# Performance work log

Measured on AMD Instinct MI355X. Metric: run time of the kernel, lower is better.

## Reference

```python
import jax, jax.numpy as jnp
import numpy as np
import math

DIM = 1024
NUM_HEADS = 16
SHARED_HEADS = 1
ROUTED_HEADS = 3
HEAD_DIM = DIM // NUM_HEADS
B, N = 2, 2048


def setup_inputs() -> dict:
    key = jax.random.key(0)
    ks = jax.random.split(key, 16)
    s = 1.0 / math.sqrt(DIM)
    inp = {
        "x": jax.random.normal(ks[0], (B, N, DIM), dtype=jnp.float32),
        "Wq": jax.random.uniform(ks[1], (DIM, DIM), minval=-s, maxval=s),
        "bq": jax.random.uniform(ks[2], (DIM,), minval=-s, maxval=s),
        "Wk": jax.random.uniform(ks[3], (DIM, DIM), minval=-s, maxval=s),
        "bk": jax.random.uniform(ks[4], (DIM,), minval=-s, maxval=s),
        "Wv": jax.random.uniform(ks[5], (DIM, DIM), minval=-s, maxval=s),
        "bv": jax.random.uniform(ks[6], (DIM,), minval=-s, maxval=s),
        "Wp": jax.random.uniform(ks[7], (DIM, DIM), minval=-s, maxval=s),
        "bp": jax.random.uniform(ks[8], (DIM,), minval=-s, maxval=s),
        "Wr": jax.random.uniform(ks[9], (NUM_HEADS - SHARED_HEADS, DIM), minval=-s, maxval=s),
        "br": jax.random.uniform(ks[10], (NUM_HEADS - SHARED_HEADS,), minval=-s, maxval=s),
        "Ws": jax.random.uniform(ks[11], (2, DIM), minval=-s, maxval=s),
        "bs": jax.random.uniform(ks[12], (2,), minval=-s, maxval=s),
        # temperature init: log(exp(1/0.24)-1), shape (H,1,1)
        "temperature": jnp.full((NUM_HEADS, 1, 1), float(np.log(np.expm1(1.0 / 0.24))), dtype=jnp.float32),
        "query_embedding": 0.02 * jax.random.normal(ks[13], (NUM_HEADS, 1, HEAD_DIM), dtype=jnp.float32),
    }
    return inp


def reference(x, Wq, bq, Wk, bk, Wv, bv, Wp, bp, Wr, br, Ws, bs, temperature, query_embedding):
    Bsz, Nn, C = x.shape
    H, hd = NUM_HEADS, HEAD_DIM

    def heads(W, b):
        y = x @ W.T + b  # [B,N,C]
        return y.reshape(Bsz, Nn, H, hd).transpose(0, 2, 1, 3)  # [B,H,N,hd]

    q = heads(Wq, bq)
    k = heads(Wk, bk)
    v = heads(Wv, bv)

    q_norm = q / jnp.linalg.norm(q, axis=-1, keepdims=True)
    q_scaled = (q_norm + query_embedding[None]) * jax.nn.softplus(temperature)[None]
    attn = jnp.einsum("bhqd,bhkd->bhqk", q_scaled, k) / math.sqrt(hd)
    attn = jax.nn.softmax(attn, axis=-1)
    h = jnp.einsum("bhqk,bhkd->bhqd", attn, v)
    h = h.transpose(0, 2, 1, 3).reshape(Bsz, Nn, C)  # [B,N,C]

    # routed-head gating
    gates = jax.nn.softmax(h @ Wr.T + br, axis=-1)  # [B,N,H-shared]
    _, idx = jax.lax.top_k(gates, ROUTED_HEADS)
    # NOTE: original uses num_classes=num_heads-shared_heads for one_hot
    mask = jax.nn.one_hot(idx, H - SHARED_HEADS, dtype=gates.dtype).sum(axis=-2)
    routed_gates = gates * mask * ROUTED_HEADS

    sw = jax.nn.softmax(h @ Ws.T + bs, axis=-1)  # [B,N,2]
    shared_gates = sw * SHARED_HEADS
    weight_0 = sw * 2.0
    shared_gates = weight_0[..., 0:1] * shared_gates
    routed_gates = weight_0[..., 1:2] * routed_gates
    masked_gates = jnp.concatenate([shared_gates, routed_gates], axis=-1)

    # einsum('bnc,bnd->bnd') == per-token scalar sum over c times h
    out = h * masked_gates.sum(axis=-1, keepdims=True)
    return out @ Wp.T + bp
```

## Files before the change

kernel.cpp:

```cpp
#include <hip/hip_runtime.h>
#include <hip/hip_bf16.h>

typedef short s16x8 __attribute__((ext_vector_type(8)));
typedef float f32x4 __attribute__((ext_vector_type(4)));

__device__ __forceinline__ float b2f(unsigned short u) {
    union { unsigned int i; float f; } v;
    v.i = ((unsigned int)u) << 16;
    return v.f;
}
__device__ __forceinline__ unsigned short f2b(float f) {
    unsigned int x = __builtin_bit_cast(unsigned int, f);
    unsigned int r = (x + 0x7fffu + ((x >> 16) & 1u)) >> 16;
    return (unsigned short)r;
}
__device__ __forceinline__ unsigned int pkbf16(float a, float b) {
    union { __hip_bfloat162 h; unsigned int u; } v;
    v.h = __float22bfloat162_rn(make_float2(a, b));
    return v.u;
}
__device__ __forceinline__ float fast_exp2(float x) { return exp2f(x); }

__device__ __forceinline__ void gl_lds16(const unsigned short* g, unsigned short* l) {
    __builtin_amdgcn_global_load_lds(
        (const __attribute__((address_space(1))) void*)g,
        (__attribute__((address_space(3))) void*)l, 16, 0, 0);
}


__device__ __forceinline__ void cvt8(const float* __restrict__ s,
                                     unsigned short* __restrict__ d, int i) {
    const float* p = s + (size_t)i * 8;
    float4 a = *(const float4*)p;
    float4 b = *(const float4*)(p + 4);
    unsigned int u0 = pkbf16(a.x, a.y), u1 = pkbf16(a.z, a.w);
    unsigned int u2 = pkbf16(b.x, b.y), u3 = pkbf16(b.z, b.w);
    uint4 o = {u0, u1, u2, u3};
    *(uint4*)&d[(size_t)i * 8] = o;
}

__global__ __launch_bounds__(256) void cvt_main(
    const float* __restrict__ x,  const float* __restrict__ Wq,
    const float* __restrict__ Wk, const float* __restrict__ Wv,
    const float* __restrict__ Wr, const float* __restrict__ Ws,
    const float* __restrict__ bq, const float* __restrict__ bk,
    const float* __restrict__ bv,
    unsigned short* __restrict__ xb, unsigned short* __restrict__ wqkv,
    unsigned short* __restrict__ wg, float* __restrict__ bqkv)
{
    int blk = blockIdx.x, t = threadIdx.x;
    if (blk < 2048)      cvt8(x,  xb,             blk * 256 + t);
    else if (blk < 2560) cvt8(Wq, wqkv,           (blk - 2048) * 256 + t);
    else if (blk < 3072) cvt8(Wk, wqkv + 1048576, (blk - 2560) * 256 + t);
    else if (blk < 3584) cvt8(Wv, wqkv + 2097152, (blk - 3072) * 256 + t);
    else if (blk < 3592) { int i = (blk - 3584) * 256 + t; if (i < 1920) cvt8(Wr, wg, i); }
    else if (blk < 3593) { int i = t; cvt8(Ws, wg + 15360, i); }
    else {
        int i = (blk - 3593) * 256 + t;
        bqkv[i] = (i < 1024) ? bq[i] : (i < 2048) ? bk[i - 1024] : bv[i - 2048];
    }
}

__global__ __launch_bounds__(256) void cvt_kernel(
    const float* __restrict__ src, unsigned short* __restrict__ dst, int n8)
{
    int i = blockIdx.x * 256 + threadIdx.x;
    if (i < n8) cvt8(src, dst, i);
}

__global__ __launch_bounds__(256) void qkv_gemm(
    const unsigned short* __restrict__ A,
    const unsigned short* __restrict__ Bw,
    const float* __restrict__ bias,
    unsigned short* __restrict__ Q, unsigned short* __restrict__ K,
    unsigned short* __restrict__ Vt)
{
    __shared__ __attribute__((aligned(16))) unsigned short As[128 * 64];
    __shared__ __attribute__((aligned(16))) unsigned short Bs[128 * 64];
    const int t = threadIdx.x;
    const int wave = t >> 6, lane = t & 63;
    const int m0 = blockIdx.x * 128, n0 = blockIdx.y * 128;
    const int wm = (wave >> 1) * 64, wn = (wave & 1) * 64;
    const int lr = lane & 15, lq = lane >> 4;
    const int srow = lane >> 3;
    const int scol = (((lane & 7) ^ srow) << 3);

    f32x4 acc[4][4];
#pragma unroll
    for (int i = 0; i < 4; ++i)
#pragma unroll
        for (int j = 0; j < 4; ++j) acc[i][j] = (f32x4){0.f, 0.f, 0.f, 0.f};

    for (int k0 = 0; k0 < 1024; k0 += 64) {
        __syncthreads();
#pragma unroll
        for (int i = 0; i < 4; ++i) {
            int rb = wave * 32 + i * 8;
            gl_lds16(&A[(size_t)(m0 + rb + srow) * 1024 + k0 + scol], &As[rb * 64]);
            gl_lds16(&Bw[(size_t)(n0 + rb + srow) * 1024 + k0 + scol], &Bs[rb * 64]);
        }
        __syncthreads();
#pragma unroll
        for (int kk = 0; kk < 64; kk += 32) {
            const int po = ((((kk >> 3) + lq) ^ (lr & 7)) << 3);
            s16x8 af[4], bf[4];
#pragma unroll
            for (int i = 0; i < 4; ++i)
                af[i] = *(const s16x8*)&As[(wm + i * 16 + lr) * 64 + po];
#pragma unroll
            for (int j = 0; j < 4; ++j)
                bf[j] = *(const s16x8*)&Bs[(wn + j * 16 + lr) * 64 + po];
#pragma unroll
            for (int i = 0; i < 4; ++i)
#pragma unroll
                for (int j = 0; j < 4; ++j)
                    acc[i][j] = __builtin_amdgcn_mfma_f32_16x16x32_bf16(af[i], bf[j], acc[i][j], 0, 0, 0);
        }
    }
    const int kind = n0 >> 10;
    const int nc = n0 & 1023;
    if (kind < 2) {
        unsigned short* Cm = kind ? K : Q;
#pragma unroll
        for (int j = 0; j < 4; ++j) {
            int cl = wn + j * 16 + lr;
            float bv = bias[n0 + cl];
#pragma unroll
            for (int i = 0; i < 4; ++i) {
                int rowb = m0 + wm + i * 16 + lq * 4;
                unsigned int u0 = pkbf16(acc[i][j][0] + bv, acc[i][j][1] + bv);
                unsigned int u1 = pkbf16(acc[i][j][2] + bv, acc[i][j][3] + bv);
                Cm[(size_t)(rowb + 0) * 1024 + nc + cl] = (unsigned short)u0;
                Cm[(size_t)(rowb + 1) * 1024 + nc + cl] = (unsigned short)(u0 >> 16);
                Cm[(size_t)(rowb + 2) * 1024 + nc + cl] = (unsigned short)u1;
                Cm[(size_t)(rowb + 3) * 1024 + nc + cl] = (unsigned short)(u1 >> 16);
            }
        }
    } else {
        const int bb = m0 >> 11;
#pragma unroll
        for (int j = 0; j < 4; ++j) {
            int col = nc + wn + j * 16 + lr;
            int hh = col >> 6, dd = col & 63;
            float bv = bias[n0 + wn + j * 16 + lr];
#pragma unroll
            for (int i = 0; i < 4; ++i) {
                int tokb = m0 + wm + i * 16 + lq * 4;
                int tloc = tokb & 2047;
                uint2 u;
                u.x = pkbf16(acc[i][j][0] + bv, acc[i][j][1] + bv);
                u.y = pkbf16(acc[i][j][2] + bv, acc[i][j][3] + bv);
                *(uint2*)&Vt[((size_t)(bb * 16 + hh) * 64 + dd) * 2048 + tloc] = u;
            }
        }
    }
}

__global__ __launch_bounds__(256) void attn_kernel(
    const unsigned short* __restrict__ Q,
    const unsigned short* __restrict__ Kb,
    const unsigned short* __restrict__ Vt,
    const float* __restrict__ temp,
    const float* __restrict__ qe,
    unsigned short* __restrict__ Hout)
{
    __shared__ __attribute__((aligned(16))) unsigned short Qs[64 * 64];
    __shared__ __attribute__((aligned(16))) unsigned short Ks[64 * 64];
    __shared__ __attribute__((aligned(16))) unsigned short Vs[64 * 64];
    __shared__ __attribute__((aligned(16))) unsigned short Ps[64 * 72];
    const int t = threadIdx.x, wave = t >> 6, lane = t & 63;
    const int lr = lane & 15, lq = lane >> 4;
    const int bh = blockIdx.y, b = bh >> 4, h = bh & 15;
    const int q0 = blockIdx.x * 64;
    const int srow = lane >> 3;
    const int scol = (((lane & 7) ^ srow) << 3);

#pragma unroll
    for (int i = 0; i < 2; ++i) {
        int rb = wave * 16 + i * 8;
        gl_lds16(&Q[(size_t)(b * 2048 + q0 + rb + srow) * 1024 + h * 64 + scol], &Qs[rb * 64]);
    }
    __syncthreads();

    {
        const int qr = t >> 2, part = t & 3;
        const int pb0 = (((part * 2) ^ (qr & 7)) << 3);
        const int pb1 = (((part * 2 + 1) ^ (qr & 7)) << 3);
        s16x8 a = *(const s16x8*)&Qs[qr * 64 + pb0];
        s16x8 c = *(const s16x8*)&Qs[qr * 64 + pb1];
        float va[8], vc[8];
        float ss = 0.f;
#pragma unroll
        for (int e = 0; e < 8; ++e) {
            va[e] = b2f((unsigned short)a[e]); vc[e] = b2f((unsigned short)c[e]);
            ss += va[e] * va[e] + vc[e] * vc[e];
        }
        ss += __shfl_xor(ss, 1); ss += __shfl_xor(ss, 2);
        float rn = rsqrtf(ss);
        float tv = temp[h];
        float sp = ((tv > 20.f) ? tv : log1pf(__expf(tv))) * 0.18033688f;
        const float* qh = qe + h * 64 + part * 16;
        s16x8 oa, oc;
#pragma unroll
        for (int e = 0; e < 8; e += 2) {
            unsigned int u0 = pkbf16((va[e] * rn + qh[e]) * sp, (va[e + 1] * rn + qh[e + 1]) * sp);
            unsigned int u1 = pkbf16((vc[e] * rn + qh[8 + e]) * sp, (vc[e + 1] * rn + qh[8 + e + 1]) * sp);
            oa[e] = (short)u0; oa[e + 1] = (short)(u0 >> 16);
            oc[e] = (short)u1; oc[e + 1] = (short)(u1 >> 16);
        }
        *(s16x8*)&Qs[qr * 64 + pb0] = oa;
        *(s16x8*)&Qs[qr * 64 + pb1] = oc;
    }

    f32x4 accO[4];
#pragma unroll
    for (int j = 0; j < 4; ++j) accO[j] = (f32x4){0.f, 0.f, 0.f, 0.f};
    float lsum[4] = {0.f, 0.f, 0.f, 0.f};

    for (int kc = 0; kc < 2048; kc += 64) {
        __syncthreads();
#pragma unroll
        for (int i = 0; i < 2; ++i) {
            int rb = wave * 16 + i * 8;
            gl_lds16(&Kb[(size_t)(b * 2048 + kc + rb + srow) * 1024 + h * 64 + scol], &Ks[rb * 64]);
            gl_lds16(&Vt[((size_t)(b * 16 + h) * 64 + rb + srow) * 2048 + kc + scol], &Vs[rb * 64]);
        }
        __syncthreads();

        f32x4 s[4];
#pragma unroll
        for (int j = 0; j < 4; ++j) s[j] = (f32x4){0.f, 0.f, 0.f, 0.f};
#pragma unroll
        for (int kk = 0; kk < 64; kk += 32) {
            const int po = ((((kk >> 3) + lq) ^ (lr & 7)) << 3);
            s16x8 aq = *(const s16x8*)&Qs[(wave * 16 + lr) * 64 + po];
#pragma unroll
            for (int j = 0; j < 4; ++j) {
                s16x8 bk = *(const s16x8*)&Ks[(j * 16 + lr) * 64 + po];
                s[j] = __builtin_amdgcn_mfma_f32_16x16x32_bf16(aq, bk, s[j], 0, 0, 0);
            }
        }

#pragma unroll
        for (int r = 0; r < 4; ++r) {
            float p0 = fast_exp2(s[0][r]), p1 = fast_exp2(s[1][r]);
            float p2 = fast_exp2(s[2][r]), p3 = fast_exp2(s[3][r]);
            lsum[r] += (p0 + p1) + (p2 + p3);
            unsigned int ua = pkbf16(p0, p1), ub = pkbf16(p2, p3);
            int base = (wave * 16 + lq * 4 + r) * 72 + lr;
            Ps[base]      = (unsigned short)ua;
            Ps[base + 16] = (unsigned short)(ua >> 16);
            Ps[base + 32] = (unsigned short)ub;
            Ps[base + 48] = (unsigned short)(ub >> 16);
        }

#pragma unroll
        for (int kk = 0; kk < 64; kk += 32) {
            const int po = ((((kk >> 3) + lq) ^ (lr & 7)) << 3);
            s16x8 ap = *(const s16x8*)&Ps[(wave * 16 + lr) * 72 + kk + lq * 8];
#pragma unroll
            for (int j = 0; j < 4; ++j) {
                s16x8 bv = *(const s16x8*)&Vs[(j * 16 + lr) * 64 + po];
                accO[j] = __builtin_amdgcn_mfma_f32_16x16x32_bf16(ap, bv, accO[j], 0, 0, 0);
            }
        }
    }

#pragma unroll
    for (int r = 0; r < 4; ++r) {
        float l = lsum[r];
        l += __shfl_xor(l, 1); l += __shfl_xor(l, 2);
        l += __shfl_xor(l, 4); l += __shfl_xor(l, 8);
        float inv = 1.f / l;
        int row = q0 + wave * 16 + lq * 4 + r;
        size_t ob = (size_t)(b * 2048 + row) * 1024 + h * 64 + lr;
        unsigned int u0 = pkbf16(accO[0][r] * inv, accO[1][r] * inv);
        unsigned int u1 = pkbf16(accO[2][r] * inv, accO[3][r] * inv);
        Hout[ob]      = (unsigned short)u0;
        Hout[ob + 16] = (unsigned short)(u0 >> 16);
        Hout[ob + 32] = (unsigned short)u1;
        Hout[ob + 48] = (unsigned short)(u1 >> 16);
    }
}

__global__ __launch_bounds__(256) void gl_gemm(
    const unsigned short* __restrict__ Hb,
    const unsigned short* __restrict__ Wg,
    float* __restrict__ logits)
{
    __shared__ __attribute__((aligned(16))) unsigned short As[128 * 64];
    __shared__ __attribute__((aligned(16))) unsigned short Gs[32 * 64];
    const int t = threadIdx.x, wave = t >> 6, lane = t & 63;
    const int lr = lane & 15, lq = lane >> 4;
    const int m0 = blockIdx.x * 128;
    const int srow = lane >> 3;
    const int scol = (((lane & 7) ^ srow) << 3);

    f32x4 acc[2][2];
#pragma unroll
    for (int i = 0; i < 2; ++i)
#pragma unroll
        for (int j = 0; j < 2; ++j) acc[i][j] = (f32x4){0.f, 0.f, 0.f, 0.f};

    for (int k0 = 0; k0 < 1024; k0 += 64) {
        __syncthreads();
#pragma unroll
        for (int i = 0; i < 4; ++i) {
            int rb = wave * 32 + i * 8;
            gl_lds16(&Hb[(size_t)(m0 + rb + srow) * 1024 + k0 + scol], &As[rb * 64]);
        }
        {
            int row = wave * 8 + srow;
            int wr = (row > 16) ? 16 : row;
            gl_lds16(&Wg[(size_t)wr * 1024 + k0 + scol], &Gs[wave * 8 * 64]);
        }
        __syncthreads();
#pragma unroll
        for (int kk = 0; kk < 64; kk += 32) {
            const int po = ((((kk >> 3) + lq) ^ (lr & 7)) << 3);
            s16x8 af[2], gf[2];
#pragma unroll
            for (int i = 0; i < 2; ++i)
                af[i] = *(const s16x8*)&As[(wave * 32 + i * 16 + lr) * 64 + po];
#pragma unroll
            for (int j = 0; j < 2; ++j)
                gf[j] = *(const s16x8*)&Gs[(j * 16 + lr) * 64 + po];
#pragma unroll
            for (int i = 0; i < 2; ++i)
#pragma unroll
                for (int j = 0; j < 2; ++j)
                    acc[i][j] = __builtin_amdgcn_mfma_f32_16x16x32_bf16(af[i], gf[j], acc[i][j], 0, 0, 0);
        }
    }
#pragma unroll
    for (int i = 0; i < 2; ++i)
#pragma unroll
        for (int j = 0; j < 2; ++j) {
            int col = j * 16 + lr;
            int rowb = m0 + wave * 32 + i * 16 + lq * 4;
#pragma unroll
            for (int r = 0; r < 4; ++r)
                logits[(size_t)(rowb + r) * 32 + col] = acc[i][j][r];
        }
}

__global__ __launch_bounds__(256) void gate_apply(
    unsigned short* __restrict__ Hb,
    const float* __restrict__ logits,
    const float* __restrict__ br,
    const float* __restrict__ bs)
{
    const int tok = blockIdx.x, t = threadIdx.x;
    float lg[17];
#pragma unroll
    for (int j = 0; j < 17; ++j)
        lg[j] = logits[(size_t)tok * 32 + j] + ((j < 15) ? br[j] : bs[j - 15]);
    float mx = lg[0];
#pragma unroll
    for (int j = 1; j < 15; ++j) mx = fmaxf(mx, lg[j]);
    float sum = 0.f, v1 = -1.f, v2 = -1.f, v3 = -1.f;
#pragma unroll
    for (int j = 0; j < 15; ++j) {
        float e = __expf(lg[j] - mx);
        sum += e;
        if (e > v1)      { v3 = v2; v2 = v1; v1 = e; }
        else if (e > v2) { v3 = v2; v2 = e; }
        else if (e > v3) { v3 = e; }
    }
    float tops = (v1 + v2 + v3) / sum;
    float sm = fmaxf(lg[15], lg[16]);
    float e0 = __expf(lg[15] - sm), e1 = __expf(lg[16] - sm);
    float inv = 1.f / (e0 + e1);
    float g = 2.f * (e0 * inv) + 6.f * (e1 * inv) * tops;

    size_t base = (size_t)tok * 1024 + t * 4;
    ushort4 hr = *(const ushort4*)&Hb[base];
    unsigned int u0 = pkbf16(b2f(hr.x) * g, b2f(hr.y) * g);
    unsigned int u1 = pkbf16(b2f(hr.z) * g, b2f(hr.w) * g);
    uint2 o = {u0, u1};
    *(uint2*)&Hb[base] = o;
}

__global__ __launch_bounds__(256) void gemm64_out(
    const unsigned short* __restrict__ A,
    const unsigned short* __restrict__ Bw,
    const float* __restrict__ bias,
    float* __restrict__ C)
{
    __shared__ __attribute__((aligned(16))) unsigned short As[64 * 64];
    __shared__ __attribute__((aligned(16))) unsigned short Bs[128 * 64];
    const int t = threadIdx.x, wave = t >> 6, lane = t & 63;
    const int lr = lane & 15, lq = lane >> 4;
    const int m0 = blockIdx.x * 64, n0 = blockIdx.y * 128;
    const int wm = (wave >> 1) * 32, wn = (wave & 1) * 64;
    const int srow = lane >> 3;
    const int scol = (((lane & 7) ^ srow) << 3);

    f32x4 acc[2][4];
#pragma unroll
    for (int i = 0; i < 2; ++i)
#pragma unroll
        for (int j = 0; j < 4; ++j) acc[i][j] = (f32x4){0.f, 0.f, 0.f, 0.f};

    for (int k0 = 0; k0 < 1024; k0 += 64) {
        __syncthreads();
#pragma unroll
        for (int i = 0; i < 2; ++i) {
            int rb = wave * 16 + i * 8;
            gl_lds16(&A[(size_t)(m0 + rb + srow) * 1024 + k0 + scol], &As[rb * 64]);
        }
#pragma unroll
        for (int i = 0; i < 4; ++i) {
            int rb = wave * 32 + i * 8;
            gl_lds16(&Bw[(size_t)(n0 + rb + srow) * 1024 + k0 + scol], &Bs[rb * 64]);
        }
        __syncthreads();
#pragma unroll
        for (int kk = 0; kk < 64; kk += 32) {
            const int po = ((((kk >> 3) + lq) ^ (lr & 7)) << 3);
            s16x8 af[2], bf[4];
#pragma unroll
            for (int i = 0; i < 2; ++i)
                af[i] = *(const s16x8*)&As[(wm + i * 16 + lr) * 64 + po];
#pragma unroll
            for (int j = 0; j < 4; ++j)
                bf[j] = *(const s16x8*)&Bs[(wn + j * 16 + lr) * 64 + po];
#pragma unroll
            for (int i = 0; i < 2; ++i)
#pragma unroll
                for (int j = 0; j < 4; ++j)
                    acc[i][j] = __builtin_amdgcn_mfma_f32_16x16x32_bf16(af[i], bf[j], acc[i][j], 0, 0, 0);
        }
    }
#pragma unroll
    for (int j = 0; j < 4; ++j) {
        int col = n0 + wn + j * 16 + lr;
        float bv = bias[col];
#pragma unroll
        for (int i = 0; i < 2; ++i) {
            int rowb = m0 + wm + i * 16 + lq * 4;
#pragma unroll
            for (int r = 0; r < 4; ++r)
                C[(size_t)(rowb + r) * 1024 + col] = acc[i][j][r] + bv;
        }
    }
}

extern "C" void kernel_launch(void* const* d_in, const int* in_sizes, int n_in,
                              void* d_out, int out_size, void* d_ws, size_t ws_size,
                              hipStream_t stream)
{
    (void)in_sizes; (void)n_in; (void)out_size; (void)ws_size;
    const float* x   = (const float*)d_in[0];
    const float* Wq  = (const float*)d_in[1];
    const float* bq  = (const float*)d_in[2];
    const float* Wk  = (const float*)d_in[3];
    const float* bk  = (const float*)d_in[4];
    const float* Wv  = (const float*)d_in[5];
    const float* bv  = (const float*)d_in[6];
    const float* Wp  = (const float*)d_in[7];
    const float* bp  = (const float*)d_in[8];
    const float* Wr  = (const float*)d_in[9];
    const float* br  = (const float*)d_in[10];
    const float* Ws  = (const float*)d_in[11];
    const float* bs  = (const float*)d_in[12];
    const float* temperature = (const float*)d_in[13];
    const float* qe  = (const float*)d_in[14];
    float* out = (float*)d_out;

    const size_t MB = 1048576;
    unsigned short* qb     = (unsigned short*)d_ws;
    unsigned short* kb     = (unsigned short*)((char*)d_ws + 8 * MB);
    unsigned short* hb     = (unsigned short*)((char*)d_ws + 16 * MB);
    unsigned short* wqkv   = (unsigned short*)((char*)d_ws + 24 * MB);
    unsigned short* wpb    = wqkv;
    unsigned short* wg     = (unsigned short*)((char*)d_ws + 30 * MB);
    float*          bqkv   = (float*)((char*)d_ws + 30 * MB + 65536);
    float*          logits = (float*)((char*)d_ws + 30 * MB + 131072);
    unsigned short* xb = (unsigned short*)d_out;
    unsigned short* vt = xb + 4 * MB;

    dim3 blk(256);
    cvt_main<<<dim3(3605), blk, 0, stream>>>(x, Wq, Wk, Wv, Wr, Ws, bq, bk, bv,
                                             xb, wqkv, wg, bqkv);
    qkv_gemm<<<dim3(32, 24), blk, 0, stream>>>(xb, wqkv, bqkv, qb, kb, vt);
    cvt_kernel<<<dim3(512), blk, 0, stream>>>(Wp, wpb, 131072);
    attn_kernel<<<dim3(32, 32), blk, 0, stream>>>(qb, kb, vt, temperature, qe, hb);
    gl_gemm<<<dim3(32), blk, 0, stream>>>(hb, wg, logits);
    gate_apply<<<dim3(4096), blk, 0, stream>>>(hb, logits, br, bs);
    gemm64_out<<<dim3(64, 8), blk, 0, stream>>>(hb, wpb, bp, out);
}
```

Before: 256.5 us.

## Double attention query tile to 128 rows per block and use native exp2

Each attention block now handles 128 query rows instead of 64, with each wave computing two 16-row fragments. Every K/V tile loaded into shared memory is therefore reused across twice as many queries, which halves K/V global traffic and the number of loads per unit of work. The cost is more registers and shared memory per block and half as many blocks (512 instead of 1024), which may lower occupancy or leave CUs underfilled. exp2f is also replaced by the AMDGPU builtin exp2 when available, which avoids the range-handling wrapper.

```diff
diff --git a/kernel.cpp b/kernel.cpp
--- a/kernel.cpp
+++ b/kernel.cpp
@@ -19,7 +19,13 @@
     v.h = __float22bfloat162_rn(make_float2(a, b));
     return v.u;
 }
-__device__ __forceinline__ float fast_exp2(float x) { return exp2f(x); }
+__device__ __forceinline__ float fast_exp2(float x) {
+#if __has_builtin(__builtin_amdgcn_exp2f)
+    return __builtin_amdgcn_exp2f(x);
+#else
+    return exp2f(x);
+#endif
+}
 
 __device__ __forceinline__ void gl_lds16(const unsigned short* g, unsigned short* l) {
     __builtin_amdgcn_global_load_lds(
@@ -164,58 +170,64 @@
     const float* __restrict__ qe,
     unsigned short* __restrict__ Hout)
 {
-    __shared__ __attribute__((aligned(16))) unsigned short Qs[64 * 64];
+    __shared__ __attribute__((aligned(16))) unsigned short Qs[128 * 64];
     __shared__ __attribute__((aligned(16))) unsigned short Ks[64 * 64];
     __shared__ __attribute__((aligned(16))) unsigned short Vs[64 * 64];
-    __shared__ __attribute__((aligned(16))) unsigned short Ps[64 * 72];
+    __shared__ __attribute__((aligned(16))) unsigned short Ps[128 * 72];
     const int t = threadIdx.x, wave = t >> 6, lane = t & 63;
     const int lr = lane & 15, lq = lane >> 4;
     const int bh = blockIdx.y, b = bh >> 4, h = bh & 15;
-    const int q0 = blockIdx.x * 64;
+    const int q0 = blockIdx.x * 128;
     const int srow = lane >> 3;
     const int scol = (((lane & 7) ^ srow) << 3);
 
 #pragma unroll
-    for (int i = 0; i < 2; ++i) {
-        int rb = wave * 16 + i * 8;
+    for (int i = 0; i < 4; ++i) {
+        int rb = wave * 32 + i * 8;
         gl_lds16(&Q[(size_t)(b * 2048 + q0 + rb + srow) * 1024 + h * 64 + scol], &Qs[rb * 64]);
     }
     __syncthreads();
 
     {
-        const int qr = t >> 2, part = t & 3;
-        const int pb0 = (((part * 2) ^ (qr & 7)) << 3);
-        const int pb1 = (((part * 2 + 1) ^ (qr & 7)) << 3);
-        s16x8 a = *(const s16x8*)&Qs[qr * 64 + pb0];
-        s16x8 c = *(const s16x8*)&Qs[qr * 64 + pb1];
-        float va[8], vc[8];
-        float ss = 0.f;
-#pragma unroll
-        for (int e = 0; e < 8; ++e) {
-            va[e] = b2f((unsigned short)a[e]); vc[e] = b2f((unsigned short)c[e]);
-            ss += va[e] * va[e] + vc[e] * vc[e];
-        }
-        ss += __shfl_xor(ss, 1); ss += __shfl_xor(ss, 2);
-        float rn = rsqrtf(ss);
+        const int qr = t >> 1, part = t & 1;
         float tv = temp[h];
         float sp = ((tv > 20.f) ? tv : log1pf(__expf(tv))) * 0.18033688f;
-        const float* qh = qe + h * 64 + part * 16;
-        s16x8 oa, oc;
-#pragma unroll
-        for (int e = 0; e < 8; e += 2) {
-            unsigned int u0 = pkbf16((va[e] * rn + qh[e]) * sp, (va[e + 1] * rn + qh[e + 1]) * sp);
-            unsigned int u1 = pkbf16((vc[e] * rn + qh[8 + e]) * sp, (vc[e + 1] * rn + qh[8 + e + 1]) * sp);
-            oa[e] = (short)u0; oa[e + 1] = (short)(u0 >> 16);
-            oc[e] = (short)u1; oc[e + 1] = (short)(u1 >> 16);
-        }
-        *(s16x8*)&Qs[qr * 64 + pb0] = oa;
-        *(s16x8*)&Qs[qr * 64 + pb1] = oc;
-    }
-
-    f32x4 accO[4];
-#pragma unroll
-    for (int j = 0; j < 4; ++j) accO[j] = (f32x4){0.f, 0.f, 0.f, 0.f};
-    float lsum[4] = {0.f, 0.f, 0.f, 0.f};
+        s16x8 frag[4];
+        float v[4][8];
+        float ss = 0.f;
+#pragma unroll
+        for (int c = 0; c < 4; ++c) {
+            int pb = (((part * 4 + c) ^ (qr & 7)) << 3);
+            frag[c] = *(const s16x8*)&Qs[qr * 64 + pb];
+#pragma unroll
+            for (int e = 0; e < 8; ++e) {
+                v[c][e] = b2f((unsigned short)frag[c][e]);
+                ss += v[c][e] * v[c][e];
+            }
+        }
+        ss += __shfl_xor(ss, 1);
+        float rn = rsqrtf(ss);
+#pragma unroll
+        for (int c = 0; c < 4; ++c) {
+            const float* qh = qe + h * 64 + (part * 4 + c) * 8;
+            s16x8 o;
+#pragma unroll
+            for (int e = 0; e < 8; e += 2) {
+                unsigned int u = pkbf16((v[c][e] * rn + qh[e]) * sp,
+                                        (v[c][e + 1] * rn + qh[e + 1]) * sp);
+                o[e] = (short)u; o[e + 1] = (short)(u >> 16);
+            }
+            int pb = (((part * 4 + c) ^ (qr & 7)) << 3);
+            *(s16x8*)&Qs[qr * 64 + pb] = o;
+        }
+    }
+
+    f32x4 accO[2][4];
+#pragma unroll
+    for (int i = 0; i < 2; ++i)
+#pragma unroll
+        for (int j = 0; j < 4; ++j) accO[i][j] = (f32x4){0.f, 0.f, 0.f, 0.f};
+    float lsum[2][4] = {{0.f, 0.f, 0.f, 0.f}, {0.f, 0.f, 0.f, 0.f}};
 
     for (int kc = 0; kc < 2048; kc += 64) {
         __syncthreads();
@@ -227,60 +239,78 @@
         }
         __syncthreads();
 
-        f32x4 s[4];
-#pragma unroll
-        for (int j = 0; j < 4; ++j) s[j] = (f32x4){0.f, 0.f, 0.f, 0.f};
+        f32x4 s[2][4];
+#pragma unroll
+        for (int i = 0; i < 2; ++i)
+#pragma unroll
+            for (int j = 0; j < 4; ++j) s[i][j] = (f32x4){0.f, 0.f, 0.f, 0.f};
 #pragma unroll
         for (int kk = 0; kk < 64; kk += 32) {
             const int po = ((((kk >> 3) + lq) ^ (lr & 7)) << 3);
-            s16x8 aq = *(const s16x8*)&Qs[(wave * 16 + lr) * 64 + po];
-#pragma unroll
-            for (int j = 0; j < 4; ++j) {
-                s16x8 bk = *(const s16x8*)&Ks[(j * 16 + lr) * 64 + po];
-                s[j] = __builtin_amdgcn_mfma_f32_16x16x32_bf16(aq, bk, s[j], 0, 0, 0);
+            s16x8 aq[2], bk[4];
+#pragma unroll
+            for (int i = 0; i < 2; ++i)
+                aq[i] = *(const s16x8*)&Qs[(wave * 32 + i * 16 + lr) * 64 + po];
+#pragma unroll
+            for (int j = 0; j < 4; ++j)
+                bk[j] = *(const s16x8*)&Ks[(j * 16 + lr) * 64 + po];
+#pragma unroll
+            for (int i = 0; i < 2; ++i)
+#pragma unroll
+                for (int j = 0; j < 4; ++j)
+                    s[i][j] = __builtin_amdgcn_mfma_f32_16x16x32_bf16(aq[i], bk[j], s[i][j], 0, 0, 0);
+        }
+
+#pragma unroll
+        for (int i = 0; i < 2; ++i)
+#pragma unroll
+            for (int r = 0; r < 4; ++r) {
+                float p0 = fast_exp2(s[i][0][r]), p1 = fast_exp2(s[i][1][r]);
+                float p2 = fast_exp2(s[i][2][r]), p3 = fast_exp2(s[i][3][r]);
+                lsum[i][r] += (p0 + p1) + (p2 + p3);
+                unsigned int ua = pkbf16(p0, p1), ub = pkbf16(p2, p3);
+                int base = (wave * 32 + i * 16 + lq * 4 + r) * 72 + lr;
+                Ps[base]      = (unsigned short)ua;
+                Ps[base + 16] = (unsigned short)(ua >> 16);
+                Ps[base + 32] = (unsigned short)ub;
+                Ps[base + 48] = (unsigned short)(ub >> 16);
             }
-        }
-
-#pragma unroll
-        for (int r = 0; r < 4; ++r) {
-            float p0 = fast_exp2(s[0][r]), p1 = fast_exp2(s[1][r]);
-            float p2 = fast_exp2(s[2][r]), p3 = fast_exp2(s[3][r]);
-            lsum[r] += (p0 + p1) + (p2 + p3);
-            unsigned int ua = pkbf16(p0, p1), ub = pkbf16(p2, p3);
-            int base = (wave * 16 + lq * 4 + r) * 72 + lr;
-            Ps[base]      = (unsigned short)ua;
-            Ps[base + 16] = (unsigned short)(ua >> 16);
-            Ps[base + 32] = (unsigned short)ub;
-            Ps[base + 48] = (unsigned short)(ub >> 16);
-        }
 
 #pragma unroll
         for (int kk = 0; kk < 64; kk += 32) {
             const int po = ((((kk >> 3) + lq) ^ (lr & 7)) << 3);
-            s16x8 ap = *(const s16x8*)&Ps[(wave * 16 + lr) * 72 + kk + lq * 8];
-#pragma unroll
-            for (int j = 0; j < 4; ++j) {
-                s16x8 bv = *(const s16x8*)&Vs[(j * 16 + lr) * 64 + po];
-                accO[j] = __builtin_amdgcn_mfma_f32_16x16x32_bf16(ap, bv, accO[j], 0, 0, 0);
-            }
-        }
-    }
-
-#pragma unroll
-    for (int r = 0; r < 4; ++r) {
-        float l = lsum[r];
-        l += __shfl_xor(l, 1); l += __shfl_xor(l, 2);
-        l += __shfl_xor(l, 4); l += __shfl_xor(l, 8);
-        float inv = 1.f / l;
-        int row = q0 + wave * 16 + lq * 4 + r;
-        size_t ob = (size_t)(b * 2048 + row) * 1024 + h * 64 + lr;
-        unsigned int u0 = pkbf16(accO[0][r] * inv, accO[1][r] * inv);
-        unsigned int u1 = pkbf16(accO[2][r] * inv, accO[3][r] * inv);
-        Hout[ob]      = (unsigned short)u0;
-        Hout[ob + 16] = (unsigned short)(u0 >> 16);
-        Hout[ob + 32] = (unsigned short)u1;
-        Hout[ob + 48] = (unsigned short)(u1 >> 16);
-    }
+            s16x8 ap[2], bv[4];
+#pragma unroll
+            for (int i = 0; i < 2; ++i)
+                ap[i] = *(const s16x8*)&Ps[(wave * 32 + i * 16 + lr) * 72 + kk + lq * 8];
+#pragma unroll
+            for (int j = 0; j < 4; ++j)
+                bv[j] = *(const s16x8*)&Vs[(j * 16 + lr) * 64 + po];
+#pragma unroll
+            for (int i = 0; i < 2; ++i)
+#pragma unroll
+                for (int j = 0; j < 4; ++j)
+                    accO[i][j] = __builtin_amdgcn_mfma_f32_16x16x32_bf16(ap[i], bv[j], accO[i][j], 0, 0, 0);
+        }
+    }
+
+#pragma unroll
+    for (int i = 0; i < 2; ++i)
+#pragma unroll
+        for (int r = 0; r < 4; ++r) {
+            float l = lsum[i][r];
+            l += __shfl_xor(l, 1); l += __shfl_xor(l, 2);
+            l += __shfl_xor(l, 4); l += __shfl_xor(l, 8);
+            float inv = 1.f / l;
+            int row = q0 + wave * 32 + i * 16 + lq * 4 + r;
+            size_t ob = (size_t)(b * 2048 + row) * 1024 + h * 64 + lr;
+            unsigned int u0 = pkbf16(accO[i][0][r] * inv, accO[i][1][r] * inv);
+            unsigned int u1 = pkbf16(accO[i][2][r] * inv, accO[i][3][r] * inv);
+            Hout[ob]      = (unsigned short)u0;
+            Hout[ob + 16] = (unsigned short)(u0 >> 16);
+            Hout[ob + 32] = (unsigned short)u1;
+            Hout[ob + 48] = (unsigned short)(u1 >> 16);
+        }
 }
 
 __global__ __launch_bounds__(256) void gl_gemm(
@@ -485,7 +515,7 @@
                                              xb, wqkv, wg, bqkv);
     qkv_gemm<<<dim3(32, 24), blk, 0, stream>>>(xb, wqkv, bqkv, qb, kb, vt);
     cvt_kernel<<<dim3(512), blk, 0, stream>>>(Wp, wpb, 131072);
-    attn_kernel<<<dim3(32, 32), blk, 0, stream>>>(qb, kb, vt, temperature, qe, hb);
+    attn_kernel<<<dim3(16, 32), blk, 0, stream>>>(qb, kb, vt, temperature, qe, hb);
     gl_gemm<<<dim3(32), blk, 0, stream>>>(hb, wg, logits);
     gate_apply<<<dim3(4096), blk, 0, stream>>>(hb, logits, br, bs);
     gemm64_out<<<dim3(64, 8), blk, 0, stream>>>(hb, wpb, bp, out);
```

Result: faster. 240.1 us (-6.4%).
